# Kernel tuning notes

Measured on AMD Instinct MI355X. Metric: run time of the kernel, lower is better.

Reference implementation:

```python
import jax, jax.numpy as jnp
import numpy as np

N_NODES = 100000
N_EDGES = 800000
D = 128   # latent feature width (node & edge)
H = 128   # MLP hidden width


def setup_inputs() -> dict:
    key = jax.random.key(0)
    ks = jax.random.split(key, 8)
    w = lambda k, shape: jax.random.normal(k, shape, jnp.float32) * 0.05
    return {
        "node_features": jax.random.normal(ks[0], (N_NODES, D), jnp.float32),
        "edge_features": jax.random.normal(ks[1], (N_EDGES, D), jnp.float32),
        "senders": jax.random.randint(ks[2], (N_EDGES,), 0, N_NODES),
        "receivers": jax.random.randint(ks[3], (N_EDGES,), 0, N_NODES),
        "We1": w(ks[4], (3 * D, H)), "be1": jnp.zeros((H,), jnp.float32),
        "We2": w(ks[5], (H, D)),     "be2": jnp.zeros((D,), jnp.float32),
        "Wn1": w(ks[6], (2 * D, H)), "bn1": jnp.zeros((H,), jnp.float32),
        "Wn2": w(ks[7], (H, D)),     "bn2": jnp.zeros((D,), jnp.float32),
    }


def _mlp(x, W1, b1, W2, b2):
    return jax.nn.relu(x @ W1 + b1) @ W2 + b2


def reference(node_features, edge_features, senders, receivers,
              We1, be1, We2, be2, Wn1, bn1, Wn2, bn2):
    # --- edge update: gather sender/receiver node feats, concat, MLP ---
    e_in = jnp.concatenate(
        [node_features[senders], node_features[receivers], edge_features], axis=-1
    )  # [E, 3D]
    e_upd = _mlp(e_in, We1, be1, We2, be2)  # [E, D]

    # --- node update: scatter-sum updated edge feats to receivers, concat, MLP ---
    agg = jax.ops.segment_sum(e_upd, receivers, num_segments=node_features.shape[0])
    n_in = jnp.concatenate([node_features, agg], axis=-1)  # [N, 2D]
    n_upd = _mlp(n_in, Wn1, bn1, Wn2, bn2)  # [N, D]

    # --- residuals ---
    new_nodes = node_features + n_upd
    new_edges = edge_features + e_upd
    return new_nodes, new_edges
```

## Files before the change

kernel.cpp:

```cpp
#include <hip/hip_runtime.h>
#include <hip/hip_bf16.h>
#include <stdint.h>

#define D 128
#define NNODES 100000
#define NEDGES 800000
#define LDSTR 136
#define EFSTR 132

typedef __bf16 bf16_t;
typedef bf16_t bf16x8 __attribute__((ext_vector_type(8)));
typedef float  f32x4  __attribute__((ext_vector_type(4)));

__global__ void wprep_kernel(const float* __restrict__ src, bf16_t* __restrict__ dst,
                             int K, int N) {
  int idx = blockIdx.x * blockDim.x + threadIdx.x;
  if (idx >= K * N) return;
  int n = idx / K;
  int k = idx - n * K;
  dst[idx] = (bf16_t)src[(size_t)k * N + n];
}

#define MFMA_CHUNK(AP, WPTR, WS, CB) do {                                        \
    _Pragma("unroll")                                                            \
    for (int kk = 0; kk < 128; kk += 32) {                                       \
      bf16x8 a[4], bb[4];                                                        \
      _Pragma("unroll")                                                          \
      for (int i = 0; i < 4; ++i) {                                              \
        float4 f0 = *(const float4*)((AP)[i] + kk + q * 8);                      \
        float4 f1 = *(const float4*)((AP)[i] + kk + q * 8 + 4);                  \
        a[i] = (bf16x8){(bf16_t)f0.x, (bf16_t)f0.y, (bf16_t)f0.z, (bf16_t)f0.w, \
                        (bf16_t)f1.x, (bf16_t)f1.y, (bf16_t)f1.z, (bf16_t)f1.w};\
      }                                                                          \
      const int kg = (CB) + kk + q * 8;                                          \
      _Pragma("unroll")                                                          \
      for (int j = 0; j < 4; ++j)                                                \
        bb[j] = *(const bf16x8*)&(WPTR)[(size_t)(n0 + j * 16 + ln) * (WS) + kg]; \
      _Pragma("unroll")                                                          \
      for (int i = 0; i < 4; ++i)                                                \
        _Pragma("unroll")                                                        \
        for (int j = 0; j < 4; ++j)                                              \
          acc[i][j] = __builtin_amdgcn_mfma_f32_16x16x32_bf16(a[i], bb[j],       \
                                                              acc[i][j], 0, 0, 0);\
    }                                                                            \
  } while (0)

__global__ __launch_bounds__(256, 3) void edge_kernel(
    const float* __restrict__ node_f, const float* __restrict__ edge_f,
    const int* __restrict__ senders, const int* __restrict__ receivers,
    const bf16_t* __restrict__ W1T,
    const float* __restrict__ be1,
    const bf16_t* __restrict__ W2T,
    const float* __restrict__ be2,
    float* __restrict__ agg,
    float* __restrict__ out_edges)
{
  __shared__ __align__(16) bf16_t Hs[128 * LDSTR];

  const int tid  = threadIdx.x;
  const int base = blockIdx.x * 128;
  const int lane = tid & 63;
  const int wave = tid >> 6;
  const int q    = lane >> 4;
  const int ln   = lane & 15;
  const int m0   = (wave & 1) * 64;
  const int n0   = (wave >> 1) * 64;

  const float* apA[4];
  const float* apB[4];
  const float* apC[4];
  #pragma unroll
  for (int i = 0; i < 4; ++i) {
    const int row = base + m0 + i * 16 + ln;
    apA[i] = node_f + (size_t)senders[row]   * D;
    apB[i] = node_f + (size_t)receivers[row] * D;
    apC[i] = edge_f + (size_t)row            * D;
  }

  f32x4 acc[4][4];
  #pragma unroll
  for (int i = 0; i < 4; i++)
    #pragma unroll
    for (int j = 0; j < 4; j++) acc[i][j] = {0.f, 0.f, 0.f, 0.f};

  MFMA_CHUNK(apA, W1T, 384, 0);
  MFMA_CHUNK(apB, W1T, 384, 128);
  MFMA_CHUNK(apC, W1T, 384, 256);

  #pragma unroll
  for (int i = 0; i < 4; i++)
    #pragma unroll
    for (int j = 0; j < 4; j++)
      #pragma unroll
      for (int r = 0; r < 4; r++) {
        int row = m0 + i * 16 + q * 4 + r;
        int col = n0 + j * 16 + ln;
        float v = acc[i][j][r] + be1[col];
        Hs[row * LDSTR + col] = (bf16_t)fmaxf(v, 0.f);
      }
  __syncthreads();

  f32x4 acc2[4][4];
  #pragma unroll
  for (int i = 0; i < 4; i++)
    #pragma unroll
    for (int j = 0; j < 4; j++) acc2[i][j] = {0.f, 0.f, 0.f, 0.f};

  #pragma unroll
  for (int kk = 0; kk < 128; kk += 32) {
    bf16x8 a[4], bb[4];
    #pragma unroll
    for (int i = 0; i < 4; i++)
      a[i] = *(const bf16x8*)&Hs[(m0 + i * 16 + ln) * LDSTR + kk + q * 8];
    #pragma unroll
    for (int j = 0; j < 4; j++)
      bb[j] = *(const bf16x8*)&W2T[(size_t)(n0 + j * 16 + ln) * 128 + kk + q * 8];
    #pragma unroll
    for (int i = 0; i < 4; i++)
      #pragma unroll
      for (int j = 0; j < 4; j++)
        acc2[i][j] = __builtin_amdgcn_mfma_f32_16x16x32_bf16(a[i], bb[j], acc2[i][j], 0, 0, 0);
  }

  float be2v[4];
  #pragma unroll
  for (int j = 0; j < 4; ++j) be2v[j] = be2[n0 + j * 16 + ln];

  int rq[4][4];
  #pragma unroll
  for (int i = 0; i < 4; ++i)
    #pragma unroll
    for (int r = 0; r < 4; ++r)
      rq[i][r] = receivers[base + m0 + i * 16 + q * 4 + r];

  #pragma unroll
  for (int i = 0; i < 4; i++)
    #pragma unroll
    for (int j = 0; j < 4; j++)
      #pragma unroll
      for (int r = 0; r < 4; r++) {
        float v = acc2[i][j][r] + be2v[j];
        acc2[i][j][r] = v;
        unsafeAtomicAdd(&agg[(size_t)rq[i][r] * D + n0 + j * 16 + ln], v);
      }

  float* Ef = (float*)Hs;
  const int lr = tid >> 2;
  const int cb = (tid & 3) * 32;
  #pragma unroll
  for (int half = 0; half < 2; ++half) {
    __syncthreads();
    if (m0 == half * 64) {
      #pragma unroll
      for (int i = 0; i < 4; i++)
        #pragma unroll
        for (int j = 0; j < 4; j++)
          #pragma unroll
          for (int r = 0; r < 4; r++)
            Ef[(i * 16 + q * 4 + r) * EFSTR + n0 + j * 16 + ln] = acc2[i][j][r];
    }
    __syncthreads();
    const size_t grow = (size_t)(base + half * 64 + lr);
    const float4* ep = (const float4*)(edge_f + grow * D + cb);
    float4*       op = (float4*)(out_edges + grow * D + cb);
    #pragma unroll
    for (int t = 0; t < 8; ++t) {
      float4 e = ep[t];
      float4 v = *(const float4*)&Ef[lr * EFSTR + cb + 4 * t];
      float4 o;
      o.x = e.x + v.x; o.y = e.y + v.y; o.z = e.z + v.z; o.w = e.w + v.w;
      op[t] = o;
    }
  }
}

__global__ __launch_bounds__(256, 3) void node_kernel(
    const float* __restrict__ node_f,
    const bf16_t* __restrict__ W1T,
    const float* __restrict__ b1,
    const bf16_t* __restrict__ W2T,
    const float* __restrict__ b2,
    const float* __restrict__ agg,
    float* __restrict__ out_nodes)
{
  __shared__ __align__(16) bf16_t Hs[128 * LDSTR];

  const int tid    = threadIdx.x;
  const int base   = blockIdx.x * 128;
  const int nvalid = min(128, NNODES - base);

  const int lane = tid & 63;
  const int wave = tid >> 6;
  const int q    = lane >> 4;
  const int ln   = lane & 15;
  const int m0   = (wave & 1) * 64;
  const int n0   = (wave >> 1) * 64;

  const float* apA[4];
  const float* apB[4];
  #pragma unroll
  for (int i = 0; i < 4; ++i) {
    const size_t row = (size_t)(base + min(m0 + i * 16 + ln, nvalid - 1));
    apA[i] = node_f + row * D;
    apB[i] = agg    + row * D;
  }

  f32x4 acc[4][4];
  #pragma unroll
  for (int i = 0; i < 4; i++)
    #pragma unroll
    for (int j = 0; j < 4; j++) acc[i][j] = {0.f, 0.f, 0.f, 0.f};

  MFMA_CHUNK(apA, W1T, 256, 0);
  MFMA_CHUNK(apB, W1T, 256, 128);

  #pragma unroll
  for (int i = 0; i < 4; i++)
    #pragma unroll
    for (int j = 0; j < 4; j++)
      #pragma unroll
      for (int r = 0; r < 4; r++) {
        int row = m0 + i * 16 + q * 4 + r;
        int col = n0 + j * 16 + ln;
        float v = acc[i][j][r] + b1[col];
        Hs[row * LDSTR + col] = (bf16_t)fmaxf(v, 0.f);
      }
  __syncthreads();

  f32x4 acc2[4][4];
  #pragma unroll
  for (int i = 0; i < 4; i++)
    #pragma unroll
    for (int j = 0; j < 4; j++) acc2[i][j] = {0.f, 0.f, 0.f, 0.f};

  #pragma unroll
  for (int kk = 0; kk < 128; kk += 32) {
    bf16x8 a[4], bb[4];
    #pragma unroll
    for (int i = 0; i < 4; i++)
      a[i] = *(const bf16x8*)&Hs[(m0 + i * 16 + ln) * LDSTR + kk + q * 8];
    #pragma unroll
    for (int j = 0; j < 4; j++)
      bb[j] = *(const bf16x8*)&W2T[(size_t)(n0 + j * 16 + ln) * 128 + kk + q * 8];
    #pragma unroll
    for (int i = 0; i < 4; i++)
      #pragma unroll
      for (int j = 0; j < 4; j++)
        acc2[i][j] = __builtin_amdgcn_mfma_f32_16x16x32_bf16(a[i], bb[j], acc2[i][j], 0, 0, 0);
  }

  float b2v[4];
  #pragma unroll
  for (int j = 0; j < 4; ++j) b2v[j] = b2[n0 + j * 16 + ln];
  #pragma unroll
  for (int i = 0; i < 4; i++)
    #pragma unroll
    for (int j = 0; j < 4; j++)
      #pragma unroll
      for (int r = 0; r < 4; r++) acc2[i][j][r] += b2v[j];

  float* Ef = (float*)Hs;
  const int lr = tid >> 2;
  const int cb = (tid & 3) * 32;
  #pragma unroll
  for (int half = 0; half < 2; ++half) {
    __syncthreads();
    if (m0 == half * 64) {
      #pragma unroll
      for (int i = 0; i < 4; i++)
        #pragma unroll
        for (int j = 0; j < 4; j++)
          #pragma unroll
          for (int r = 0; r < 4; r++)
            Ef[(i * 16 + q * 4 + r) * EFSTR + n0 + j * 16 + ln] = acc2[i][j][r];
    }
    __syncthreads();
    const size_t grow = (size_t)(base + half * 64 + lr);
    if (grow < NNODES) {
      const float4* np = (const float4*)(node_f + grow * D + cb);
      float4*       op = (float4*)(out_nodes + grow * D + cb);
      #pragma unroll
      for (int t = 0; t < 8; ++t) {
        float4 n = np[t];
        float4 v = *(const float4*)&Ef[lr * EFSTR + cb + 4 * t];
        float4 o;
        o.x = n.x + v.x; o.y = n.y + v.y; o.z = n.z + v.z; o.w = n.w + v.w;
        op[t] = o;
      }
    }
  }
}

extern "C" void kernel_launch(void* const* d_in, const int* in_sizes, int n_in,
                              void* d_out, int out_size, void* d_ws, size_t ws_size,
                              hipStream_t stream) {
  const float* node_f    = (const float*)d_in[0];
  const float* edge_f    = (const float*)d_in[1];
  const int*   senders   = (const int*)d_in[2];
  const int*   receivers = (const int*)d_in[3];
  const float* We1 = (const float*)d_in[4];
  const float* be1 = (const float*)d_in[5];
  const float* We2 = (const float*)d_in[6];
  const float* be2 = (const float*)d_in[7];
  const float* Wn1 = (const float*)d_in[8];
  const float* bn1 = (const float*)d_in[9];
  const float* Wn2 = (const float*)d_in[10];
  const float* bn2 = (const float*)d_in[11];

  float* out_nodes = (float*)d_out;
  float* out_edges = out_nodes + (size_t)NNODES * D;

  bf16_t* W1T  = (bf16_t*)d_ws;
  bf16_t* W2T  = W1T  + 128 * 384;
  bf16_t* Wn1T = W2T  + 128 * 128;
  bf16_t* Wn2T = Wn1T + 128 * 256;

  hipMemsetAsync(d_out, 0, (size_t)NNODES * D * sizeof(float), stream);

  wprep_kernel<<<(384 * 128 + 255) / 256, 256, 0, stream>>>(We1, W1T, 384, 128);
  wprep_kernel<<<(128 * 128 + 255) / 256, 256, 0, stream>>>(We2, W2T, 128, 128);
  wprep_kernel<<<(256 * 128 + 255) / 256, 256, 0, stream>>>(Wn1, Wn1T, 256, 128);
  wprep_kernel<<<(128 * 128 + 255) / 256, 256, 0, stream>>>(Wn2, Wn2T, 128, 128);

  edge_kernel<<<NEDGES / 128, 256, 0, stream>>>(
      node_f, edge_f, senders, receivers, W1T, be1, W2T, be2, out_nodes, out_edges);

  node_kernel<<<(NNODES + 127) / 128, 256, 0, stream>>>(
      node_f, Wn1T, bn1, Wn2T, bn2, out_nodes, out_nodes);
}
```

Before: 1.414 ms.

## Stage edge-kernel gathers into LDS with async global_load_lds triple buffering

The edge kernel's first GEMM no longer reads gathered sender, receiver and edge rows directly from global memory into registers. It issues asynchronous global-to-LDS loads into a three-slot ring buffer, XOR-swizzled to avoid bank conflicts, and prefetches two chunks ahead with explicit vmcnt waits and barriers. The goal is to hide gather latency behind MFMA work and cut the duplicated global reads across waves that share rows. In exchange, LDS use grows to 48KB per block, which may limit occupancy, and two barriers per chunk are added.

```diff
diff --git a/kernel.cpp b/kernel.cpp
--- a/kernel.cpp
+++ b/kernel.cpp
@@ -11,6 +11,13 @@
 typedef __bf16 bf16_t;
 typedef bf16_t bf16x8 __attribute__((ext_vector_type(8)));
 typedef float  f32x4  __attribute__((ext_vector_type(4)));
+
+typedef __attribute__((address_space(3))) void       lds_void;
+typedef __attribute__((address_space(1))) const void glb_void;
+
+__device__ __forceinline__ void gld_lds16(const void* g, void* l) {
+  __builtin_amdgcn_global_load_lds((glb_void*)g, (lds_void*)l, 16, 0, 0);
+}
 
 __global__ void wprep_kernel(const float* __restrict__ src, bf16_t* __restrict__ dst,
                              int K, int N) {
@@ -20,30 +27,6 @@
   int k = idx - n * K;
   dst[idx] = (bf16_t)src[(size_t)k * N + n];
 }
-
-#define MFMA_CHUNK(AP, WPTR, WS, CB) do {                                        \
-    _Pragma("unroll")                                                            \
-    for (int kk = 0; kk < 128; kk += 32) {                                       \
-      bf16x8 a[4], bb[4];                                                        \
-      _Pragma("unroll")                                                          \
-      for (int i = 0; i < 4; ++i) {                                              \
-        float4 f0 = *(const float4*)((AP)[i] + kk + q * 8);                      \
-        float4 f1 = *(const float4*)((AP)[i] + kk + q * 8 + 4);                  \
-        a[i] = (bf16x8){(bf16_t)f0.x, (bf16_t)f0.y, (bf16_t)f0.z, (bf16_t)f0.w, \
-                        (bf16_t)f1.x, (bf16_t)f1.y, (bf16_t)f1.z, (bf16_t)f1.w};\
-      }                                                                          \
-      const int kg = (CB) + kk + q * 8;                                          \
-      _Pragma("unroll")                                                          \
-      for (int j = 0; j < 4; ++j)                                                \
-        bb[j] = *(const bf16x8*)&(WPTR)[(size_t)(n0 + j * 16 + ln) * (WS) + kg]; \
-      _Pragma("unroll")                                                          \
-      for (int i = 0; i < 4; ++i)                                                \
-        _Pragma("unroll")                                                        \
-        for (int j = 0; j < 4; ++j)                                              \
-          acc[i][j] = __builtin_amdgcn_mfma_f32_16x16x32_bf16(a[i], bb[j],       \
-                                                              acc[i][j], 0, 0, 0);\
-    }                                                                            \
-  } while (0)
 
 __global__ __launch_bounds__(256, 3) void edge_kernel(
     const float* __restrict__ node_f, const float* __restrict__ edge_f,
@@ -55,7 +38,7 @@
     float* __restrict__ agg,
     float* __restrict__ out_edges)
 {
-  __shared__ __align__(16) bf16_t Hs[128 * LDSTR];
+  __shared__ __align__(16) char smem[49152];
 
   const int tid  = threadIdx.x;
   const int base = blockIdx.x * 128;
@@ -66,15 +49,20 @@
   const int m0   = (wave & 1) * 64;
   const int n0   = (wave >> 1) * 64;
 
-  const float* apA[4];
-  const float* apB[4];
-  const float* apC[4];
-  #pragma unroll
-  for (int i = 0; i < 4; ++i) {
-    const int row = base + m0 + i * 16 + ln;
-    apA[i] = node_f + (size_t)senders[row]   * D;
-    apB[i] = node_f + (size_t)receivers[row] * D;
-    apC[i] = edge_f + (size_t)row            * D;
+  const int sRow8 = lane >> 3;
+  const int slot  = lane & 7;
+
+  int        rowq[4];
+  const float* srcSnd[4];
+  const float* srcRcv[4];
+  const float* srcEdg[4];
+  #pragma unroll
+  for (int s = 0; s < 4; ++s) {
+    const int r = (wave * 4 + s) * 8 + sRow8;
+    rowq[s]   = r;
+    srcSnd[s] = node_f + (size_t)senders[base + r]   * D;
+    srcRcv[s] = node_f + (size_t)receivers[base + r] * D;
+    srcEdg[s] = edge_f + (size_t)(base + r)          * D;
   }
 
   f32x4 acc[4][4];
@@ -83,10 +71,65 @@
     #pragma unroll
     for (int j = 0; j < 4; j++) acc[i][j] = {0.f, 0.f, 0.f, 0.f};
 
-  MFMA_CHUNK(apA, W1T, 384, 0);
-  MFMA_CHUNK(apB, W1T, 384, 128);
-  MFMA_CHUNK(apC, W1T, 384, 256);
-
+#define STAGE_E(HC) do {                                                        \
+    const int sel_ = (HC) >> 2, kq_ = (HC) & 3;                                 \
+    char* bufb_ = smem + ((HC) % 3) * 16384;                                    \
+    _Pragma("unroll")                                                           \
+    for (int s = 0; s < 4; ++s) {                                               \
+      const float* srow_ = (sel_ == 0) ? srcSnd[s]                              \
+                         : (sel_ == 1) ? srcRcv[s] : srcEdg[s];                 \
+      const void* g_ = (const char*)srow_ + kq_ * 128                           \
+                       + ((slot ^ (rowq[s] & 7)) << 4);                         \
+      void* l_ = bufb_ + (wave * 4 + s) * 1024;          \
+      gld_lds16(g_, l_);                                                        \
+    }                                                                           \
+  } while (0)
+
+#define COMPUTE_E(HC) do {                                                      \
+    const int sel_ = (HC) >> 2, kq_ = (HC) & 3;                                 \
+    const char* bufb_ = smem + ((HC) % 3) * 16384;                              \
+    bf16x8 a_[4], bb_[4];                                                       \
+    _Pragma("unroll")                                                           \
+    for (int i = 0; i < 4; ++i) {                                               \
+      const int r_ = m0 + i * 16 + ln;                                          \
+      const int e_ = r_ & 7;                                                    \
+      const char* rb_ = bufb_ + r_ * 128;                                       \
+      f32x4 lo_ = *(const f32x4*)(rb_ + (((2 * q)     ^ e_) << 4));             \
+      f32x4 hi_ = *(const f32x4*)(rb_ + (((2 * q + 1) ^ e_) << 4));             \
+      a_[i] = (bf16x8){(bf16_t)lo_[0], (bf16_t)lo_[1], (bf16_t)lo_[2],          \
+                       (bf16_t)lo_[3], (bf16_t)hi_[0], (bf16_t)hi_[1],          \
+                       (bf16_t)hi_[2], (bf16_t)hi_[3]};                         \
+    }                                                                           \
+    const int kg_ = sel_ * 128 + kq_ * 32 + q * 8;                              \
+    _Pragma("unroll")                                                           \
+    for (int j = 0; j < 4; ++j)                                                 \
+      bb_[j] = *(const bf16x8*)&W1T[(size_t)(n0 + j * 16 + ln) * 384 + kg_];    \
+    _Pragma("unroll")                                                           \
+    for (int i = 0; i < 4; ++i)                                                 \
+      _Pragma("unroll")                                                         \
+      for (int j = 0; j < 4; ++j)                                               \
+        acc[i][j] = __builtin_amdgcn_mfma_f32_16x16x32_bf16(a_[i], bb_[j],      \
+                                                            acc[i][j], 0, 0, 0);\
+  } while (0)
+
+#define PHASE_E(HC, NW) do {                                                    \
+    if ((HC) + 2 < 12) STAGE_E((HC) + 2);                                       \
+    asm volatile("s_waitcnt vmcnt(" #NW ")" ::: "memory");                      \
+    __builtin_amdgcn_s_barrier();                                               \
+    __builtin_amdgcn_sched_barrier(0);                                          \
+    COMPUTE_E(HC);                                                              \
+    __builtin_amdgcn_sched_barrier(0);                                          \
+    __builtin_amdgcn_s_barrier();                                               \
+    __builtin_amdgcn_sched_barrier(0);                                          \
+  } while (0)
+
+  STAGE_E(0);
+  STAGE_E(1);
+  PHASE_E(0, 8);  PHASE_E(1, 8);  PHASE_E(2, 8);  PHASE_E(3, 8);
+  PHASE_E(4, 8);  PHASE_E(5, 8);  PHASE_E(6, 8);  PHASE_E(7, 8);
+  PHASE_E(8, 8);  PHASE_E(9, 8);  PHASE_E(10, 4); PHASE_E(11, 0);
+
+  bf16_t* Hs = (bf16_t*)smem;
   #pragma unroll
   for (int i = 0; i < 4; i++)
     #pragma unroll
@@ -144,7 +187,7 @@
         unsafeAtomicAdd(&agg[(size_t)rq[i][r] * D + n0 + j * 16 + ln], v);
       }
 
-  float* Ef = (float*)Hs;
+  float* Ef = (float*)smem;
   const int lr = tid >> 2;
   const int cb = (tid & 3) * 32;
   #pragma unroll
@@ -172,6 +215,9 @@
       op[t] = o;
     }
   }
+#undef STAGE_E
+#undef COMPUTE_E
+#undef PHASE_E
 }
 
 __global__ __launch_bounds__(256, 3) void node_kernel(
@@ -211,8 +257,32 @@
     #pragma unroll
     for (int j = 0; j < 4; j++) acc[i][j] = {0.f, 0.f, 0.f, 0.f};
 
-  MFMA_CHUNK(apA, W1T, 256, 0);
-  MFMA_CHUNK(apB, W1T, 256, 128);
+#define MFMA_CHUNK_N(AP, CB) do {                                               \
+    _Pragma("unroll")                                                           \
+    for (int kk = 0; kk < 128; kk += 32) {                                      \
+      bf16x8 a[4], bb[4];                                                       \
+      _Pragma("unroll")                                                         \
+      for (int i = 0; i < 4; ++i) {                                             \
+        float4 f0 = *(const float4*)((AP)[i] + kk + q * 8);                     \
+        float4 f1 = *(const float4*)((AP)[i] + kk + q * 8 + 4);                 \
+        a[i] = (bf16x8){(bf16_t)f0.x, (bf16_t)f0.y, (bf16_t)f0.z, (bf16_t)f0.w,\
+                        (bf16_t)f1.x, (bf16_t)f1.y, (bf16_t)f1.z, (bf16_t)f1.w};\
+      }                                                                         \
+      const int kg = (CB) + kk + q * 8;                                         \
+      _Pragma("unroll")                                                         \
+      for (int j = 0; j < 4; ++j)                                               \
+        bb[j] = *(const bf16x8*)&W1T[(size_t)(n0 + j * 16 + ln) * 256 + kg];    \
+      _Pragma("unroll")                                                         \
+      for (int i = 0; i < 4; ++i)                                               \
+        _Pragma("unroll")                                                       \
+        for (int j = 0; j < 4; ++j)                                             \
+          acc[i][j] = __builtin_amdgcn_mfma_f32_16x16x32_bf16(a[i], bb[j],      \
+                                                              acc[i][j], 0, 0, 0);\
+    }                                                                           \
+  } while (0)
+
+  MFMA_CHUNK_N(apA, 0);
+  MFMA_CHUNK_N(apB, 128);
 
   #pragma unroll
   for (int i = 0; i < 4; i++)
@@ -289,6 +359,7 @@
       }
     }
   }
+#undef MFMA_CHUNK_N
 }
 
 extern "C" void kernel_launch(void* const* d_in, const int* in_sizes, int n_in,
```

Result: faster. 1.243 ms (-12.1%).
